# Kernel optimization log

Hardware: AMD Instinct MI355X
Metric: run time of the kernel (lower is better)

The kernel has to match this reference:

```python
import jax, jax.numpy as jnp
import numpy as np

# Model/config dims
U, B, D, H, R, S, M = 512, 16, 512, 8, 32, 16, 32
HD = D // H
Q = R + U + S          # query length
KV = M + R + U         # key/value length
PE = 2 * U - 1         # relative position embedding length (training mode)
NEG_INF = -1e8
SCALE = HD ** -0.5


def setup_inputs() -> dict:
    key = jax.random.key(0)
    ks = jax.random.split(key, 14)
    f = lambda k, shp: jax.random.normal(k, shp, dtype=jnp.float32)
    return {
        "utterance": f(ks[0], (U, B, D)),
        "lengths": jax.random.randint(ks[1], (B,), U // 2, U + 1),
        "right_context": f(ks[2], (R, B, D)),
        "summary": f(ks[3], (S, B, D)),
        "memory": f(ks[4], (M, B, D)),
        "attention_mask": jax.random.bernoulli(ks[5], 0.5, (Q, KV)),  # True = masked
        "pos_emb": f(ks[6], (PE, D)),
        "Wq": f(ks[7], (D, D)) * 0.02, "bq": jnp.zeros((D,), jnp.float32),
        "Wkv": f(ks[8], (2 * D, D)) * 0.02, "bkv": jnp.zeros((2 * D,), jnp.float32),
        "Wo": f(ks[9], (D, D)) * 0.02, "bo": jnp.zeros((D,), jnp.float32),
        "Wpos": f(ks[10], (D, D)) * 0.02,
        "pos_bias_u": f(ks[11], (H, HD)) * 0.02,
        "pos_bias_v": f(ks[12], (H, HD)) * 0.02,
    }


def _rel_shift(x):
    # x: (B, H, U, PE) -> (B, H, U, PE - U + 1); out[..., u, j] = x[..., u, (U-1) - u + j]
    b, h, u, pe = x.shape
    out_len = pe - (u - 1)
    idx = (u - 1) - jnp.arange(u)[:, None] + jnp.arange(out_len)[None, :]  # (U, out_len)
    return jnp.take_along_axis(x, idx[None, None], axis=3)


def reference(utterance, lengths, right_context, summary, memory, attention_mask,
              pos_emb, Wq, bq, Wkv, bkv, Wo, bo, Wpos, pos_bias_u, pos_bias_v):
    # Projections
    query = jnp.concatenate([right_context, utterance, summary]) @ Wq.T + bq      # (Q, B, D)
    kv = jnp.concatenate([memory, right_context, utterance]) @ Wkv.T + bkv        # (KV, B, 2D)
    key_t, val_t = jnp.split(kv, 2, axis=2)                                       # (KV, B, D) each

    rk = key_t.reshape(KV, B * H, HD).transpose(1, 0, 2)                          # (B*H, KV, HD)
    rv = val_t.reshape(KV, B * H, HD).transpose(1, 0, 2)
    q4 = query.reshape(Q, B, H, HD)

    # content term (matrix AC) with pos_bias_u
    qu = (q4 + pos_bias_u).reshape(Q, B * H, HD).transpose(1, 0, 2)               # (B*H, Q, HD)
    matrix_ac = jnp.einsum('nqd,nkd->nqk', qu, rk)                                # (B*H, Q, KV)

    # positional term (matrix BD) with pos_bias_v, only for utterance queries
    uv = (q4[R:R + U] + pos_bias_v).transpose(1, 2, 0, 3)                         # (B, H, U, HD)
    pos = (pos_emb @ Wpos.T).reshape(PE, H, HD).transpose(1, 0, 2)                # (H, PE, HD)
    bd = jnp.einsum('bhud,hpd->bhup', uv, pos)                                    # (B, H, U, PE)
    bd = _rel_shift(bd).reshape(B * H, U, -1)                                     # (B*H, U, U)
    matrix_bd = jnp.zeros_like(matrix_ac).at[:, R:R + U, M + R:].set(bd)

    w = (matrix_ac + matrix_bd) * SCALE
    w = jnp.where(attention_mask[None], NEG_INF, w)
    # padding mask (B > 1 branch): pad positions where kv index >= KV - U + lengths
    pad = jnp.arange(KV)[None, :] >= (KV - U + lengths)[:, None]                  # (B, KV)
    w = jnp.where(pad[:, None, None, :], NEG_INF, w.reshape(B, H, Q, KV)).reshape(B * H, Q, KV)

    probs = jax.nn.softmax(w, axis=-1)
    attn = jnp.einsum('nqk,nkd->nqd', probs, rv)                                  # (B*H, Q, HD)
    attn = attn.transpose(1, 0, 2).reshape(Q, B, D)
    outputs = attn @ Wo.T + bo

    out_right_context_utterance = outputs[:R + U]                                 # (R+U, B, D)
    out_memory = jnp.clip(outputs[R + U:], -10.0, 10.0)                           # (S, B, D), tanh_on_mem=False
    return out_right_context_utterance, out_memory, key_t, val_t
```

## Files before the change

### kernel.cpp

```cpp
#include <hip/hip_runtime.h>
#include <math.h>


#define NEG_INF_F (-100000000.0f)
#define SCALE_F   (0.125f)

typedef short  short8 __attribute__((ext_vector_type(8)));
typedef float  f32x4  __attribute__((ext_vector_type(4)));
typedef unsigned short u16x4 __attribute__((ext_vector_type(4)));
typedef unsigned short u16x8 __attribute__((ext_vector_type(8)));

__device__ __forceinline__ unsigned short f2b(float f) {
    unsigned int u = __builtin_bit_cast(unsigned int, f);
    u = u + 0x7FFFu + ((u >> 16) & 1u);
    return (unsigned short)(u >> 16);
}
__device__ __forceinline__ float b2f(unsigned short h) {
    unsigned int u = ((unsigned int)h) << 16;
    return __builtin_bit_cast(float, u);
}

__device__ __forceinline__ int swzK(int row, int colB) {
    return row * 64 + ((colB ^ ((row & 7) << 4)) >> 1);
}
__device__ __forceinline__ int swzS(int row, int colB) {
    return row * 576 + ((colB ^ ((row & 7) << 4)) >> 1);
}

__global__ __launch_bounds__(256) void detect_mask_kernel(
    const unsigned int* __restrict__ m, int nwords, int* __restrict__ flags) {
    __shared__ int fF, fG;
    if (threadIdx.x == 0) { fF = 0; fG = 0; }
    __syncthreads();
    int lF = 0, lG = 0;
    for (int i = blockIdx.x * 256 + threadIdx.x; i < nwords; i += gridDim.x * 256) {
        unsigned int w = m[i];
        if (w == 0x3F800000u)      lF = 1;
        else if (w > 1u)           lG = 1;
    }
    if (lF) atomicOr(&fF, 1);
    if (lG) atomicOr(&fG, 1);
    __syncthreads();
    if (threadIdx.x == 0) {
        if (fF) atomicOr(&flags[0], 1);
        if (fG) atomicOr(&flags[1], 1);
    }
}

__global__ __launch_bounds__(256) void maskprep_kernel(
    const void* __restrict__ maskPtr, const int* __restrict__ flags,
    const int* __restrict__ lengths,
    unsigned short* __restrict__ maskBias, unsigned short* __restrict__ padBias)
{
    const int mode = flags[0] ? 2 : (flags[1] ? 1 : 0);
    const unsigned short NB = f2b(NEG_INF_F);
    for (int i = blockIdx.x * 256 + threadIdx.x; i < 560 * 576; i += gridDim.x * 256) {
        bool m;
        if (mode == 1)      m = ((const unsigned char*)maskPtr)[i] != 0;
        else if (mode == 2) m = ((const float*)maskPtr)[i] != 0.f;
        else                m = ((const int*)maskPtr)[i] != 0;
        maskBias[i] = m ? NB : (unsigned short)0;
    }
    for (int i = blockIdx.x * 256 + threadIdx.x; i < 16 * 576; i += gridDim.x * 256) {
        int b = i / 576, k = i - b * 576;
        padBias[i] = (k >= 64 + lengths[b]) ? NB : (unsigned short)0;
    }
}

__global__ __launch_bounds__(256) void conv9_kernel(
    const float* s0, const float* s1, const float* s2, const float* s3,
    const float* s4, const float* s5, const float* s6, const float* s7,
    const float* s8,
    unsigned short* d0, unsigned short* d1, unsigned short* d2,
    unsigned short* d3, unsigned short* d4, unsigned short* d5,
    unsigned short* d6, unsigned short* d7, unsigned short* d8,
    int n0, int n1, int n2, int n3, int n4, int n5, int n6, int n7, int n8)
{
    const float* ss[9] = {s0, s1, s2, s3, s4, s5, s6, s7, s8};
    unsigned short* dd[9] = {d0, d1, d2, d3, d4, d5, d6, d7, d8};
    int nn[9] = {n0, n1, n2, n3, n4, n5, n6, n7, n8};
    const int a = blockIdx.y;
    const float* s = ss[a];
    unsigned short* d = dd[a];
    const int nq = nn[a] >> 2;
    for (int i = blockIdx.x * 256 + threadIdx.x; i < nq; i += gridDim.x * 256) {
        float4 v = *(const float4*)(s + (size_t)i * 4);
        u16x4 o = {f2b(v.x), f2b(v.y), f2b(v.z), f2b(v.w)};
        *(u16x4*)(d + (size_t)i * 4) = o;
    }
}

struct GemmJob {
    const unsigned short *a0, *a1, *a2;
    int rb1, rb2, Mrows;
    const unsigned short *Wt;
    const float *bias;
    float *out0, *out1;
    unsigned short *auxU, *auxV;
    const float *pbu, *pbv;
    int mode, clampStart;
    int nBlocks;
    int base;
};

__global__ __launch_bounds__(256) void gemm_mfma3(GemmJob J0, GemmJob J1, GemmJob J2)
{
    __shared__ __attribute__((aligned(16))) unsigned short As[128 * 64];
    __shared__ __attribute__((aligned(16))) unsigned short Ws[128 * 64];

    const int bid = blockIdx.x;
    GemmJob J;
    if (bid >= J2.base)      J = J2;
    else if (bid >= J1.base) J = J1;
    else                     J = J0;
    const int rel = bid - J.base;
    const int bn = (rel % J.nBlocks) * 128;
    const int bm = (rel / J.nBlocks) * 128;

    const int tid = threadIdx.x;
    const int w = tid >> 6, lane = tid & 63;
    const int l15 = lane & 15, l4 = lane >> 4;
    const int wm = (w & 1) * 64, wn = (w >> 1) * 64;

    const int lrow  = lane >> 3;
    const int lslot = lane & 7;
    const int swzS16 = (lslot ^ lrow) * 8;

    const unsigned short* srcA[4];
    const unsigned short* srcW[4];
    #pragma unroll
    for (int c = 0; c < 4; ++c) {
        const int row = w * 32 + c * 8 + lrow;
        const int r = bm + row;
        const unsigned short* s;
        if (r < J.rb1)      s = J.a0 + (size_t)r * 512;
        else if (r < J.rb2) s = J.a1 + (size_t)(r - J.rb1) * 512;
        else                s = J.a2 + (size_t)(r - J.rb2) * 512;
        srcA[c] = s + swzS16;
        srcW[c] = J.Wt + (size_t)(bn + row) * 512 + swzS16;
    }

    f32x4 acc[4][4];
    #pragma unroll
    for (int i = 0; i < 4; ++i)
        #pragma unroll
        for (int j = 0; j < 4; ++j) acc[i][j] = (f32x4){0.f, 0.f, 0.f, 0.f};

    #define GFRAG(arr, row, kk) \
        (*(const short8*)&arr[(row) * 64 + ((((kk) * 4 + l4) ^ ((row) & 7)) * 8)])

    for (int kt = 0; kt < 8; ++kt) {
        __syncthreads();
        #pragma unroll
        for (int c = 0; c < 4; ++c) {
            __builtin_amdgcn_global_load_lds(
                (const __attribute__((address_space(1))) unsigned int*)(srcA[c] + kt * 64),
                (__attribute__((address_space(3))) unsigned int*)&As[(w * 32 + c * 8) * 64],
                16, 0, 0);
            __builtin_amdgcn_global_load_lds(
                (const __attribute__((address_space(1))) unsigned int*)(srcW[c] + kt * 64),
                (__attribute__((address_space(3))) unsigned int*)&Ws[(w * 32 + c * 8) * 64],
                16, 0, 0);
        }
        __syncthreads();

        short8 bfr[4][2];
        #pragma unroll
        for (int t = 0; t < 4; ++t) {
            const int r = wn + t * 16 + l15;
            bfr[t][0] = GFRAG(Ws, r, 0);
            bfr[t][1] = GFRAG(Ws, r, 1);
        }
        #pragma unroll
        for (int tm = 0; tm < 4; ++tm) {
            const int r = wm + tm * 16 + l15;
            const short8 a0f = GFRAG(As, r, 0);
            const short8 a1f = GFRAG(As, r, 1);
            #pragma unroll
            for (int tn = 0; tn < 4; ++tn) {
                acc[tm][tn] = __builtin_amdgcn_mfma_f32_16x16x32_bf16(
                    a0f, bfr[tn][0], acc[tm][tn], 0, 0, 0);
                acc[tm][tn] = __builtin_amdgcn_mfma_f32_16x16x32_bf16(
                    a1f, bfr[tn][1], acc[tm][tn], 0, 0, 0);
            }
        }
    }
    #undef GFRAG

    #pragma unroll
    for (int tm = 0; tm < 4; ++tm) {
        #pragma unroll
        for (int tn = 0; tn < 4; ++tn) {
            const int col = bn + wn + tn * 16 + l15;
            const float bv = J.bias ? J.bias[col] : 0.f;
            #pragma unroll
            for (int rr = 0; rr < 4; ++rr) {
                const int row = bm + wm + tm * 16 + l4 * 4 + rr;
                if (row >= J.Mrows) continue;
                float v = acc[tm][tn][rr] + bv;
                if (J.mode == 0) {
                    if (row >= J.clampStart) v = fminf(fmaxf(v, -10.f), 10.f);
                    J.out0[(size_t)row * 512 + col] = v;
                } else if (J.mode == 1) {
                    int bb = row & 15, kv = row >> 4;
                    if (col < 512) {
                        J.out0[(size_t)row * 512 + col] = v;
                        int hh = col >> 6, hd = col & 63;
                        J.auxU[(((size_t)(bb * 8 + hh)) * 576 + kv) * 64 + hd] = f2b(v);
                    } else {
                        J.out1[(size_t)row * 512 + (col - 512)] = v;
                        int cc = col - 512, hh = cc >> 6, hd = cc & 63;
                        J.auxV[(((size_t)(bb * 8 + hh)) * 64 + hd) * 576 + kv] = f2b(v);
                    }
                } else if (J.mode == 2) {
                    int q = row >> 4, bb = row & 15, hh = col >> 6, hd = col & 63;
                    size_t base = (((size_t)(bb * 8 + hh)) * 576 + q) * 64 + hd;
                    J.auxU[base] = f2b((v + J.pbu[col]) * SCALE_F);
                    J.auxV[base] = f2b((v + J.pbv[col]) * SCALE_F);
                } else {
                    int hh = col >> 6, hd = col & 63;
                    J.auxU[((size_t)hh * 1023 + row) * 64 + hd] = f2b(v);
                }
            }
        }
    }
}

__global__ __launch_bounds__(256) void attn_mfma_kernel(
    const unsigned short* __restrict__ Qu_g,
    const unsigned short* __restrict__ Qv_g,
    const unsigned short* __restrict__ K_g,
    const unsigned short* __restrict__ VT_g,
    const unsigned short* __restrict__ P_g,
    const unsigned short* __restrict__ maskBias,
    const unsigned short* __restrict__ padBias,
    unsigned short* __restrict__ attnT)
{
    __shared__ __attribute__((aligned(16))) unsigned short sc[32 * 576];
    __shared__ __attribute__((aligned(16))) unsigned short stg[2 * 4096];
    __shared__ float rowv[32];

    const int bid = blockIdx.y * 18 + blockIdx.x;
    const int workid = (bid & 7) * 288 + (bid >> 3);
    const int n = workid / 18;
    const int qt = workid - n * 18;

    const int b = n >> 3, h = n & 7;
    const int q0 = qt * 32;
    const int tid = threadIdx.x;
    const int w = tid >> 6, lane = tid & 63;
    const int l15 = lane & 15, l4 = lane >> 4;
    const int mT = (w >> 1) * 16;
    const int c0 = (w & 1) * 32;
    const int t0base = 16 - mT + c0;
    const bool hasBand = (qt >= 1 && qt <= 16);
    const int pbq = 512 - q0;

    const unsigned short* Kn  = K_g  + (size_t)n * 576 * 64;
    const unsigned short* VTn = VT_g + (size_t)n * 64 * 576;
    const unsigned short* Ph  = P_g  + (size_t)h * 1023 * 64;

    const int srow  = tid >> 3;
    const int sIdx  = (tid & 7) * 8;
    const int scolB = sIdx * 2;

    {
        u16x8 a = *(const u16x8*)&Kn[(size_t)srow * 64 + sIdx];
        u16x8 c = *(const u16x8*)&Kn[(size_t)(srow + 32) * 64 + sIdx];
        *(u16x8*)&stg[swzK(srow, scolB)] = a;
        *(u16x8*)&stg[swzK(srow + 32, scolB)] = c;
    }

    short8 quf[2], qvf[2];
    {
        size_t rb = ((size_t)n * 576 + q0 + mT + l15) * 64;
        quf[0] = *(const short8*)&Qu_g[rb + l4 * 8];
        quf[1] = *(const short8*)&Qu_g[rb + 32 + l4 * 8];
        qvf[0] = *(const short8*)&Qv_g[rb + l4 * 8];
        qvf[1] = *(const short8*)&Qv_g[rb + 32 + l4 * 8];
    }

    int cur = 0;
    for (int kt = 0; kt < 9; ++kt) {
        u16x8 kna, knb;
        if (kt < 8) {
            kna = *(const u16x8*)&Kn[(size_t)((kt + 1) * 64 + srow) * 64 + sIdx];
            knb = *(const u16x8*)&Kn[(size_t)((kt + 1) * 64 + srow + 32) * 64 + sIdx];
        }
        const bool doBand = hasBand && (kt >= 1);
        short8 bnd00, bnd01, bnd10, bnd11, bnd20, bnd21;
        if (doBand) {
            const int pbase = pbq + (kt - 1) * 64 + t0base + l15;
            int p0 = pbase;       p0 = p0 < 0 ? 0 : (p0 > 1022 ? 1022 : p0);
            int p1 = pbase + 16;  p1 = p1 < 0 ? 0 : (p1 > 1022 ? 1022 : p1);
            int p2 = pbase + 32;  p2 = p2 < 0 ? 0 : (p2 > 1022 ? 1022 : p2);
            bnd00 = *(const short8*)&Ph[(size_t)p0 * 64 + l4 * 8];
            bnd01 = *(const short8*)&Ph[(size_t)p0 * 64 + 32 + l4 * 8];
            bnd10 = *(const short8*)&Ph[(size_t)p1 * 64 + l4 * 8];
            bnd11 = *(const short8*)&Ph[(size_t)p1 * 64 + 32 + l4 * 8];
            bnd20 = *(const short8*)&Ph[(size_t)p2 * 64 + l4 * 8];
            bnd21 = *(const short8*)&Ph[(size_t)p2 * 64 + 32 + l4 * 8];
        }
        __syncthreads();
        unsigned short* buf = stg + cur * 4096;
        __builtin_amdgcn_s_setprio(1);
        #pragma unroll
        for (int s = 0; s < 2; ++s) {
            const int n0 = c0 + s * 16;
            f32x4 acc = {0.f, 0.f, 0.f, 0.f};
            short8 b0 = *(const short8*)&buf[swzK(n0 + l15, l4 * 16)];
            short8 b1 = *(const short8*)&buf[swzK(n0 + l15, 64 + l4 * 16)];
            acc = __builtin_amdgcn_mfma_f32_16x16x32_bf16(quf[0], b0, acc, 0, 0, 0);
            acc = __builtin_amdgcn_mfma_f32_16x16x32_bf16(quf[1], b1, acc, 0, 0, 0);
            const int col = kt * 64 + n0 + l15;
            #pragma unroll
            for (int r = 0; r < 4; ++r)
                sc[swzS(mT + l4 * 4 + r, col * 2)] = f2b(acc[r]);
        }
        __builtin_amdgcn_s_setprio(0);
        if (doBand) {
            #pragma unroll
            for (int s = 0; s < 3; ++s) {
                short8 ba = (s == 0) ? bnd00 : ((s == 1) ? bnd10 : bnd20);
                short8 bb = (s == 0) ? bnd01 : ((s == 1) ? bnd11 : bnd21);
                f32x4 acc = {0.f, 0.f, 0.f, 0.f};
                acc = __builtin_amdgcn_mfma_f32_16x16x32_bf16(qvf[0], ba, acc, 0, 0, 0);
                acc = __builtin_amdgcn_mfma_f32_16x16x32_bf16(qvf[1], bb, acc, 0, 0, 0);
                const int tl = t0base + s * 16 + l15;
                #pragma unroll
                for (int r = 0; r < 4; ++r) {
                    const int du = mT + l4 * 4 + r;
                    const int dj = tl - 31 + du;
                    if (dj >= c0 && dj < c0 + 32) {
                        const int ix = swzS(du, (kt * 64 + dj) * 2);
                        sc[ix] = f2b(b2f(sc[ix]) + acc[r]);
                    }
                }
            }
        }
        if (kt < 8) {
            unsigned short* nb = stg + (cur ^ 1) * 4096;
            *(u16x8*)&nb[swzK(srow, scolB)] = kna;
            *(u16x8*)&nb[swzK(srow + 32, scolB)] = knb;
        }
        cur ^= 1;
    }

    u16x8 va = *(const u16x8*)&VTn[(size_t)srow * 576 + sIdx];
    u16x8 vb = *(const u16x8*)&VTn[(size_t)(srow + 32) * 576 + sIdx];
    __syncthreads();

    {
        const int row = tid >> 3, seg = tid & 7;
        const int q = q0 + row;
        const int qc = q < 560 ? q : 559;
        const unsigned short* mb  = maskBias + (size_t)qc * 576 + seg * 72;
        const unsigned short* pbb = padBias + (size_t)b * 576 + seg * 72;
        float mx = -3.0e38f;
        #pragma unroll
        for (int ci = 0; ci < 9; ++ci) {
            u16x8 sv = *(const u16x8*)&sc[swzS(row, seg * 144 + ci * 16)];
            u16x8 mv = *(const u16x8*)&mb[ci * 8];
            u16x8 pv = *(const u16x8*)&pbb[ci * 8];
            #pragma unroll
            for (int j = 0; j < 8; ++j)
                mx = fmaxf(mx, b2f(sv[j]) + b2f(mv[j]) + b2f(pv[j]));
        }
        mx = fmaxf(mx, __shfl_xor(mx, 1));
        mx = fmaxf(mx, __shfl_xor(mx, 2));
        mx = fmaxf(mx, __shfl_xor(mx, 4));
        float lsum = 0.f;
        #pragma unroll
        for (int ci = 0; ci < 9; ++ci) {
            const int ix = swzS(row, seg * 144 + ci * 16);
            u16x8 sv = *(const u16x8*)&sc[ix];
            u16x8 mv = *(const u16x8*)&mb[ci * 8];
            u16x8 pv = *(const u16x8*)&pbb[ci * 8];
            u16x8 ev;
            #pragma unroll
            for (int j = 0; j < 8; ++j) {
                float e = __expf(b2f(sv[j]) + b2f(mv[j]) + b2f(pv[j]) - mx);
                ev[j] = f2b(e); lsum += e;
            }
            *(u16x8*)&sc[ix] = ev;
        }
        lsum += __shfl_xor(lsum, 1);
        lsum += __shfl_xor(lsum, 2);
        lsum += __shfl_xor(lsum, 4);
        if (seg == 0) rowv[row] = 1.f / lsum;
    }
    *(u16x8*)&stg[swzK(srow, scolB)] = va;
    *(u16x8*)&stg[swzK(srow + 32, scolB)] = vb;

    f32x4 oacc0 = {0.f, 0.f, 0.f, 0.f}, oacc1 = {0.f, 0.f, 0.f, 0.f};
    cur = 0;
    for (int kt = 0; kt < 9; ++kt) {
        u16x8 vna, vnb;
        if (kt < 8) {
            vna = *(const u16x8*)&VTn[(size_t)srow * 576 + (kt + 1) * 64 + sIdx];
            vnb = *(const u16x8*)&VTn[(size_t)(srow + 32) * 576 + (kt + 1) * 64 + sIdx];
        }
        __syncthreads();
        unsigned short* buf = stg + cur * 4096;
        short8 af0 = *(const short8*)&sc[swzS(mT + l15, kt * 128 + l4 * 16)];
        short8 af1 = *(const short8*)&sc[swzS(mT + l15, kt * 128 + 64 + l4 * 16)];
        __builtin_amdgcn_s_setprio(1);
        {
            short8 b00 = *(const short8*)&buf[swzK(c0 + l15, l4 * 16)];
            short8 b01 = *(const short8*)&buf[swzK(c0 + l15, 64 + l4 * 16)];
            short8 b10 = *(const short8*)&buf[swzK(c0 + 16 + l15, l4 * 16)];
            short8 b11 = *(const short8*)&buf[swzK(c0 + 16 + l15, 64 + l4 * 16)];
            oacc0 = __builtin_amdgcn_mfma_f32_16x16x32_bf16(af0, b00, oacc0, 0, 0, 0);
            oacc0 = __builtin_amdgcn_mfma_f32_16x16x32_bf16(af1, b01, oacc0, 0, 0, 0);
            oacc1 = __builtin_amdgcn_mfma_f32_16x16x32_bf16(af0, b10, oacc1, 0, 0, 0);
            oacc1 = __builtin_amdgcn_mfma_f32_16x16x32_bf16(af1, b11, oacc1, 0, 0, 0);
        }
        __builtin_amdgcn_s_setprio(0);
        if (kt < 8) {
            unsigned short* nb = stg + (cur ^ 1) * 4096;
            *(u16x8*)&nb[swzK(srow, scolB)] = vna;
            *(u16x8*)&nb[swzK(srow + 32, scolB)] = vnb;
        }
        cur ^= 1;
    }

    #pragma unroll
    for (int s = 0; s < 2; ++s) {
        const f32x4 oa = s ? oacc1 : oacc0;
        const int n0 = c0 + s * 16;
        #pragma unroll
        for (int r = 0; r < 4; ++r) {
            const int row = mT + l4 * 4 + r, q = q0 + row;
            if (q < 560)
                attnT[((size_t)q * 16 + b) * 512 + h * 64 + n0 + l15] =
                    f2b(oa[r] * rowv[row]);
        }
    }
}

extern "C" void kernel_launch(void* const* d_in, const int* in_sizes, int n_in,
                              void* d_out, int out_size, void* d_ws, size_t ws_size,
                              hipStream_t stream) {
    const float* utt     = (const float*)d_in[0];
    const int*   lengths = (const int*)d_in[1];
    const float* rc      = (const float*)d_in[2];
    const float* summ    = (const float*)d_in[3];
    const float* mem     = (const float*)d_in[4];
    const void*  mask    = d_in[5];
    const float* pos_emb = (const float*)d_in[6];
    const float* Wq      = (const float*)d_in[7];
    const float* bq      = (const float*)d_in[8];
    const float* Wkv     = (const float*)d_in[9];
    const float* bkv     = (const float*)d_in[10];
    const float* Wo      = (const float*)d_in[11];
    const float* bo      = (const float*)d_in[12];
    const float* Wpos    = (const float*)d_in[13];
    const float* pbu     = (const float*)d_in[14];
    const float* pbv     = (const float*)d_in[15];

    float* out = (float*)d_out;
    float* out0   = out;
    float* keyOut = out + 4587520;
    float* valOut = out + 9306112;

    int* flags = (int*)d_ws;
    unsigned short* U = (unsigned short*)d_ws + 64;
    unsigned short* utt_bf  = U;
    unsigned short* rc_bf   = utt_bf  + 4194304;
    unsigned short* summ_bf = rc_bf   + 262144;
    unsigned short* mem_bf  = summ_bf + 131072;
    unsigned short* pose_bf = mem_bf  + 262144;
    unsigned short* wq_bf   = pose_bf + 523776;
    unsigned short* wkv_bf  = wq_bf   + 262144;
    unsigned short* wo_bf   = wkv_bf  + 524288;
    unsigned short* wpos_bf = wo_bf   + 262144;
    unsigned short* Qu_bf   = wpos_bf + 262144;
    unsigned short* Qv_bf   = Qu_bf   + 4718592;
    unsigned short* K_bf    = Qv_bf   + 4718592;
    unsigned short* VT_bf   = K_bf    + 4718592;
    unsigned short* posW_bf = VT_bf   + 4718592;
    unsigned short* attnT_bf= posW_bf + 523776;
    unsigned short* maskB   = attnT_bf + 4587520;
    unsigned short* padB    = maskB + 322560;

    hipMemsetAsync(flags, 0, 2 * sizeof(int), stream);
    detect_mask_kernel<<<158, 256, 0, stream>>>((const unsigned int*)mask,
                                                (560 * 576) / 4, flags);
    maskprep_kernel<<<315, 256, 0, stream>>>(mask, flags, lengths, maskB, padB);

    conv9_kernel<<<dim3(1024, 9), 256, 0, stream>>>(
        utt, rc, summ, mem, pos_emb, Wq, Wkv, Wo, Wpos,
        utt_bf, rc_bf, summ_bf, mem_bf, pose_bf, wq_bf, wkv_bf, wo_bf, wpos_bf,
        4194304, 262144, 131072, 262144, 523776, 262144, 524288, 262144, 262144);

    GemmJob jq;
    jq.a0 = rc_bf; jq.a1 = utt_bf; jq.a2 = summ_bf;
    jq.rb1 = 512; jq.rb2 = 8704; jq.Mrows = 8960;
    jq.Wt = wq_bf; jq.bias = bq;
    jq.out0 = nullptr; jq.out1 = nullptr;
    jq.auxU = Qu_bf; jq.auxV = Qv_bf;
    jq.pbu = pbu; jq.pbv = pbv;
    jq.mode = 2; jq.clampStart = 0; jq.nBlocks = 4; jq.base = 0;

    GemmJob jkv;
    jkv.a0 = mem_bf; jkv.a1 = rc_bf; jkv.a2 = utt_bf;
    jkv.rb1 = 512; jkv.rb2 = 1024; jkv.Mrows = 9216;
    jkv.Wt = wkv_bf; jkv.bias = bkv;
    jkv.out0 = keyOut; jkv.out1 = valOut;
    jkv.auxU = K_bf; jkv.auxV = VT_bf;
    jkv.pbu = nullptr; jkv.pbv = nullptr;
    jkv.mode = 1; jkv.clampStart = 0; jkv.nBlocks = 8; jkv.base = 280;

    GemmJob jp;
    jp.a0 = pose_bf; jp.a1 = pose_bf; jp.a2 = pose_bf;
    jp.rb1 = 1 << 30; jp.rb2 = 1 << 30; jp.Mrows = 1023;
    jp.Wt = wpos_bf; jp.bias = nullptr;
    jp.out0 = nullptr; jp.out1 = nullptr;
    jp.auxU = posW_bf; jp.auxV = nullptr;
    jp.pbu = nullptr; jp.pbv = nullptr;
    jp.mode = 3; jp.clampStart = 0; jp.nBlocks = 4; jp.base = 856;

    gemm_mfma3<<<888, 256, 0, stream>>>(jq, jkv, jp);

    attn_mfma_kernel<<<dim3(18, 128), 256, 0, stream>>>(
        Qu_bf, Qv_bf, K_bf, VT_bf, posW_bf, maskB, padB, attnT_bf);

    GemmJob jo;
    jo.a0 = attnT_bf; jo.a1 = attnT_bf; jo.a2 = attnT_bf;
    jo.rb1 = 1 << 30; jo.rb2 = 1 << 30; jo.Mrows = 8960;
    jo.Wt = wo_bf; jo.bias = bo;
    jo.out0 = out0; jo.out1 = nullptr;
    jo.auxU = nullptr; jo.auxV = nullptr;
    jo.pbu = nullptr; jo.pbv = nullptr;
    jo.mode = 0; jo.clampStart = 8704; jo.nBlocks = 4; jo.base = 0;

    GemmJob jdummy = jo;
    jdummy.base = 1 << 30;

    gemm_mfma3<<<280, 256, 0, stream>>>(jo, jdummy, jdummy);
}
```

Measured before the change: 303.8 us.

## Fold mask kernels into conv and GEMM launches; read K/V fragments directly from global

Mask-type detection now runs as an extra y-slice of the conversion kernel, and mask/pad bias prep runs as extra tail blocks of the projection GEMM launch. This removes two separate kernel launches and their serialization. The attention kernel drops its double-buffered LDS staging of K and V^T and loads MFMA B-fragments straight from global memory. That removes the per-tile barriers and the LDS traffic, but adds uncoalesced, cache-dependent global reads.

```diff
diff --git a/kernel.cpp b/kernel.cpp
--- a/kernel.cpp
+++ b/kernel.cpp
@@ -20,51 +20,8 @@
     return __builtin_bit_cast(float, u);
 }
 
-__device__ __forceinline__ int swzK(int row, int colB) {
-    return row * 64 + ((colB ^ ((row & 7) << 4)) >> 1);
-}
 __device__ __forceinline__ int swzS(int row, int colB) {
     return row * 576 + ((colB ^ ((row & 7) << 4)) >> 1);
-}
-
-__global__ __launch_bounds__(256) void detect_mask_kernel(
-    const unsigned int* __restrict__ m, int nwords, int* __restrict__ flags) {
-    __shared__ int fF, fG;
-    if (threadIdx.x == 0) { fF = 0; fG = 0; }
-    __syncthreads();
-    int lF = 0, lG = 0;
-    for (int i = blockIdx.x * 256 + threadIdx.x; i < nwords; i += gridDim.x * 256) {
-        unsigned int w = m[i];
-        if (w == 0x3F800000u)      lF = 1;
-        else if (w > 1u)           lG = 1;
-    }
-    if (lF) atomicOr(&fF, 1);
-    if (lG) atomicOr(&fG, 1);
-    __syncthreads();
-    if (threadIdx.x == 0) {
-        if (fF) atomicOr(&flags[0], 1);
-        if (fG) atomicOr(&flags[1], 1);
-    }
-}
-
-__global__ __launch_bounds__(256) void maskprep_kernel(
-    const void* __restrict__ maskPtr, const int* __restrict__ flags,
-    const int* __restrict__ lengths,
-    unsigned short* __restrict__ maskBias, unsigned short* __restrict__ padBias)
-{
-    const int mode = flags[0] ? 2 : (flags[1] ? 1 : 0);
-    const unsigned short NB = f2b(NEG_INF_F);
-    for (int i = blockIdx.x * 256 + threadIdx.x; i < 560 * 576; i += gridDim.x * 256) {
-        bool m;
-        if (mode == 1)      m = ((const unsigned char*)maskPtr)[i] != 0;
-        else if (mode == 2) m = ((const float*)maskPtr)[i] != 0.f;
-        else                m = ((const int*)maskPtr)[i] != 0;
-        maskBias[i] = m ? NB : (unsigned short)0;
-    }
-    for (int i = blockIdx.x * 256 + threadIdx.x; i < 16 * 576; i += gridDim.x * 256) {
-        int b = i / 576, k = i - b * 576;
-        padBias[i] = (k >= 64 + lengths[b]) ? NB : (unsigned short)0;
-    }
 }
 
 __global__ __launch_bounds__(256) void conv9_kernel(
@@ -74,12 +31,32 @@
     unsigned short* d0, unsigned short* d1, unsigned short* d2,
     unsigned short* d3, unsigned short* d4, unsigned short* d5,
     unsigned short* d6, unsigned short* d7, unsigned short* d8,
-    int n0, int n1, int n2, int n3, int n4, int n5, int n6, int n7, int n8)
+    int n0, int n1, int n2, int n3, int n4, int n5, int n6, int n7, int n8,
+    const unsigned int* __restrict__ mask, int nwords, int* __restrict__ flags)
 {
+    __shared__ int fF, fG;
+    const int a = blockIdx.y;
+    if (a == 9) {
+        if (threadIdx.x == 0) { fF = 0; fG = 0; }
+        __syncthreads();
+        int lF = 0, lG = 0;
+        for (int i = blockIdx.x * 256 + threadIdx.x; i < nwords; i += gridDim.x * 256) {
+            unsigned int w = mask[i];
+            if (w == 0x3F800000u)      lF = 1;
+            else if (w > 1u)           lG = 1;
+        }
+        if (lF) atomicOr(&fF, 1);
+        if (lG) atomicOr(&fG, 1);
+        __syncthreads();
+        if (threadIdx.x == 0) {
+            if (fF) atomicOr(&flags[0], 1);
+            if (fG) atomicOr(&flags[1], 1);
+        }
+        return;
+    }
     const float* ss[9] = {s0, s1, s2, s3, s4, s5, s6, s7, s8};
     unsigned short* dd[9] = {d0, d1, d2, d3, d4, d5, d6, d7, d8};
     int nn[9] = {n0, n1, n2, n3, n4, n5, n6, n7, n8};
-    const int a = blockIdx.y;
     const float* s = ss[a];
     unsigned short* d = dd[a];
     const int nq = nn[a] >> 2;
@@ -103,12 +80,36 @@
     int base;
 };
 
-__global__ __launch_bounds__(256) void gemm_mfma3(GemmJob J0, GemmJob J1, GemmJob J2)
+__global__ __launch_bounds__(256) void gemm_mfma3(
+    GemmJob J0, GemmJob J1, GemmJob J2,
+    const void* __restrict__ maskPtr, const int* __restrict__ flags,
+    const int* __restrict__ lengths,
+    unsigned short* __restrict__ maskB, unsigned short* __restrict__ padB,
+    int maskBase)
 {
     __shared__ __attribute__((aligned(16))) unsigned short As[128 * 64];
     __shared__ __attribute__((aligned(16))) unsigned short Ws[128 * 64];
 
     const int bid = blockIdx.x;
+    if (bid >= maskBase) {
+        const int mode = flags[0] ? 2 : (flags[1] ? 1 : 0);
+        const unsigned short NB = f2b(NEG_INF_F);
+        const int nBlk = gridDim.x - maskBase;
+        const int stride = nBlk * 256;
+        for (int i = (bid - maskBase) * 256 + threadIdx.x; i < 560 * 576; i += stride) {
+            bool m;
+            if (mode == 1)      m = ((const unsigned char*)maskPtr)[i] != 0;
+            else if (mode == 2) m = ((const float*)maskPtr)[i] != 0.f;
+            else                m = ((const int*)maskPtr)[i] != 0;
+            maskB[i] = m ? NB : (unsigned short)0;
+        }
+        for (int i = (bid - maskBase) * 256 + threadIdx.x; i < 16 * 576; i += stride) {
+            int b = i / 576, k = i - b * 576;
+            padB[i] = (k >= 64 + lengths[b]) ? NB : (unsigned short)0;
+        }
+        return;
+    }
+
     GemmJob J;
     if (bid >= J2.base)      J = J2;
     else if (bid >= J1.base) J = J1;
@@ -237,7 +238,6 @@
     unsigned short* __restrict__ attnT)
 {
     __shared__ __attribute__((aligned(16))) unsigned short sc[32 * 576];
-    __shared__ __attribute__((aligned(16))) unsigned short stg[2 * 4096];
     __shared__ float rowv[32];
 
     const int bid = blockIdx.y * 18 + blockIdx.x;
@@ -260,17 +260,6 @@
     const unsigned short* VTn = VT_g + (size_t)n * 64 * 576;
     const unsigned short* Ph  = P_g  + (size_t)h * 1023 * 64;
 
-    const int srow  = tid >> 3;
-    const int sIdx  = (tid & 7) * 8;
-    const int scolB = sIdx * 2;
-
-    {
-        u16x8 a = *(const u16x8*)&Kn[(size_t)srow * 64 + sIdx];
-        u16x8 c = *(const u16x8*)&Kn[(size_t)(srow + 32) * 64 + sIdx];
-        *(u16x8*)&stg[swzK(srow, scolB)] = a;
-        *(u16x8*)&stg[swzK(srow + 32, scolB)] = c;
-    }
-
     short8 quf[2], qvf[2];
     {
         size_t rb = ((size_t)n * 576 + q0 + mT + l15) * 64;
@@ -280,13 +269,7 @@
         qvf[1] = *(const short8*)&Qv_g[rb + 32 + l4 * 8];
     }
 
-    int cur = 0;
     for (int kt = 0; kt < 9; ++kt) {
-        u16x8 kna, knb;
-        if (kt < 8) {
-            kna = *(const u16x8*)&Kn[(size_t)((kt + 1) * 64 + srow) * 64 + sIdx];
-            knb = *(const u16x8*)&Kn[(size_t)((kt + 1) * 64 + srow + 32) * 64 + sIdx];
-        }
         const bool doBand = hasBand && (kt >= 1);
         short8 bnd00, bnd01, bnd10, bnd11, bnd20, bnd21;
         if (doBand) {
@@ -301,15 +284,14 @@
             bnd20 = *(const short8*)&Ph[(size_t)p2 * 64 + l4 * 8];
             bnd21 = *(const short8*)&Ph[(size_t)p2 * 64 + 32 + l4 * 8];
         }
-        __syncthreads();
-        unsigned short* buf = stg + cur * 4096;
         __builtin_amdgcn_s_setprio(1);
         #pragma unroll
         for (int s = 0; s < 2; ++s) {
             const int n0 = c0 + s * 16;
+            const unsigned short* kp = Kn + (size_t)(kt * 64 + n0 + l15) * 64;
+            short8 b0 = *(const short8*)&kp[l4 * 8];
+            short8 b1 = *(const short8*)&kp[32 + l4 * 8];
             f32x4 acc = {0.f, 0.f, 0.f, 0.f};
-            short8 b0 = *(const short8*)&buf[swzK(n0 + l15, l4 * 16)];
-            short8 b1 = *(const short8*)&buf[swzK(n0 + l15, 64 + l4 * 16)];
             acc = __builtin_amdgcn_mfma_f32_16x16x32_bf16(quf[0], b0, acc, 0, 0, 0);
             acc = __builtin_amdgcn_mfma_f32_16x16x32_bf16(quf[1], b1, acc, 0, 0, 0);
             const int col = kt * 64 + n0 + l15;
@@ -317,7 +299,6 @@
             for (int r = 0; r < 4; ++r)
                 sc[swzS(mT + l4 * 4 + r, col * 2)] = f2b(acc[r]);
         }
-        __builtin_amdgcn_s_setprio(0);
         if (doBand) {
             #pragma unroll
             for (int s = 0; s < 3; ++s) {
@@ -338,16 +319,8 @@
                 }
             }
         }
-        if (kt < 8) {
-            unsigned short* nb = stg + (cur ^ 1) * 4096;
-            *(u16x8*)&nb[swzK(srow, scolB)] = kna;
-            *(u16x8*)&nb[swzK(srow + 32, scolB)] = knb;
-        }
-        cur ^= 1;
-    }
-
-    u16x8 va = *(const u16x8*)&VTn[(size_t)srow * 576 + sIdx];
-    u16x8 vb = *(const u16x8*)&VTn[(size_t)(srow + 32) * 576 + sIdx];
+        __builtin_amdgcn_s_setprio(0);
+    }
     __syncthreads();
 
     {
@@ -389,39 +362,24 @@
         lsum += __shfl_xor(lsum, 4);
         if (seg == 0) rowv[row] = 1.f / lsum;
     }
-    *(u16x8*)&stg[swzK(srow, scolB)] = va;
-    *(u16x8*)&stg[swzK(srow + 32, scolB)] = vb;
+    __syncthreads();
 
     f32x4 oacc0 = {0.f, 0.f, 0.f, 0.f}, oacc1 = {0.f, 0.f, 0.f, 0.f};
-    cur = 0;
     for (int kt = 0; kt < 9; ++kt) {
-        u16x8 vna, vnb;
-        if (kt < 8) {
-            vna = *(const u16x8*)&VTn[(size_t)srow * 576 + (kt + 1) * 64 + sIdx];
-            vnb = *(const u16x8*)&VTn[(size_t)(srow + 32) * 576 + (kt + 1) * 64 + sIdx];
-        }
-        __syncthreads();
-        unsigned short* buf = stg + cur * 4096;
+        const unsigned short* vp0 = VTn + (size_t)(c0 + l15) * 576 + kt * 64;
+        const unsigned short* vp1 = VTn + (size_t)(c0 + 16 + l15) * 576 + kt * 64;
+        short8 b00 = *(const short8*)&vp0[l4 * 8];
+        short8 b01 = *(const short8*)&vp0[32 + l4 * 8];
+        short8 b10 = *(const short8*)&vp1[l4 * 8];
+        short8 b11 = *(const short8*)&vp1[32 + l4 * 8];
         short8 af0 = *(const short8*)&sc[swzS(mT + l15, kt * 128 + l4 * 16)];
         short8 af1 = *(const short8*)&sc[swzS(mT + l15, kt * 128 + 64 + l4 * 16)];
         __builtin_amdgcn_s_setprio(1);
-        {
-            short8 b00 = *(const short8*)&buf[swzK(c0 + l15, l4 * 16)];
-            short8 b01 = *(const short8*)&buf[swzK(c0 + l15, 64 + l4 * 16)];
-            short8 b10 = *(const short8*)&buf[swzK(c0 + 16 + l15, l4 * 16)];
-            short8 b11 = *(const short8*)&buf[swzK(c0 + 16 + l15, 64 + l4 * 16)];
-            oacc0 = __builtin_amdgcn_mfma_f32_16x16x32_bf16(af0, b00, oacc0, 0, 0, 0);
-            oacc0 = __builtin_amdgcn_mfma_f32_16x16x32_bf16(af1, b01, oacc0, 0, 0, 0);
-            oacc1 = __builtin_amdgcn_mfma_f32_16x16x32_bf16(af0, b10, oacc1, 0, 0, 0);
-            oacc1 = __builtin_amdgcn_mfma_f32_16x16x32_bf16(af1, b11, oacc1, 0, 0, 0);
-        }
+        oacc0 = __builtin_amdgcn_mfma_f32_16x16x32_bf16(af0, b00, oacc0, 0, 0, 0);
+        oacc0 = __builtin_amdgcn_mfma_f32_16x16x32_bf16(af1, b01, oacc0, 0, 0, 0);
+        oacc1 = __builtin_amdgcn_mfma_f32_16x16x32_bf16(af0, b10, oacc1, 0, 0, 0);
+        oacc1 = __builtin_amdgcn_mfma_f32_16x16x32_bf16(af1, b11, oacc1, 0, 0, 0);
         __builtin_amdgcn_s_setprio(0);
-        if (kt < 8) {
-            unsigned short* nb = stg + (cur ^ 1) * 4096;
-            *(u16x8*)&nb[swzK(srow, scolB)] = vna;
-            *(u16x8*)&nb[swzK(srow + 32, scolB)] = vnb;
-        }
-        cur ^= 1;
     }
 
     #pragma unroll
@@ -484,14 +442,12 @@
     unsigned short* padB    = maskB + 322560;
 
     hipMemsetAsync(flags, 0, 2 * sizeof(int), stream);
-    detect_mask_kernel<<<158, 256, 0, stream>>>((const unsigned int*)mask,
-                                                (560 * 576) / 4, flags);
-    maskprep_kernel<<<315, 256, 0, stream>>>(mask, flags, lengths, maskB, padB);
-
-    conv9_kernel<<<dim3(1024, 9), 256, 0, stream>>>(
+
+    conv9_kernel<<<dim3(1024, 10), 256, 0, stream>>>(
         utt, rc, summ, mem, pos_emb, Wq, Wkv, Wo, Wpos,
         utt_bf, rc_bf, summ_bf, mem_bf, pose_bf, wq_bf, wkv_bf, wo_bf, wpos_bf,
-        4194304, 262144, 131072, 262144, 523776, 262144, 524288, 262144, 262144);
+        4194304, 262144, 131072, 262144, 523776, 262144, 524288, 262144, 262144,
+        (const unsigned int*)mask, (560 * 576) / 4, flags);
 
     GemmJob jq;
     jq.a0 = rc_bf; jq.a1 = utt_bf; jq.a2 = summ_bf;
@@ -520,7 +476,8 @@
     jp.pbu = nullptr; jp.pbv = nullptr;
     jp.mode = 3; jp.clampStart = 0; jp.nBlocks = 4; jp.base = 856;
 
-    gemm_mfma3<<<888, 256, 0, stream>>>(jq, jkv, jp);
+    gemm_mfma3<<<952, 256, 0, stream>>>(jq, jkv, jp,
+        mask, flags, lengths, maskB, padB, 888);
 
     attn_mfma_kernel<<<dim3(18, 128), 256, 0, stream>>>(
         Qu_bf, Qv_bf, K_bf, VT_bf, posW_bf, maskB, padB, attnT_bf);
@@ -537,5 +494,6 @@
     GemmJob jdummy = jo;
     jdummy.base = 1 << 30;
 
-    gemm_mfma3<<<280, 256, 0, stream>>>(jo, jdummy, jdummy);
-}
+    gemm_mfma3<<<280, 256, 0, stream>>>(jo, jdummy, jdummy,
+        mask, flags, lengths, maskB, padB, 1 << 30);
+}
```

Result: slower. 356.4 us (+17.3%).
